# Kernel tuning notes

Hardware: AMD Instinct MI355X
Metric: run time of the kernel (lower is better)

The kernel has to match this reference:

```python
import jax, jax.numpy as jnp
import numpy as np

B, N, F, W = 8, 2048, 128, 64


def setup_inputs() -> dict:
    key = jax.random.key(0)
    k1, k2, k3, k4 = jax.random.split(key, 4)
    x = jax.random.normal(k1, (B, N, F), dtype=jnp.float32)
    adj = jnp.ones((B, N, N), dtype=bool)  # accepted by forward but unused
    w_key = jax.random.normal(k2, (F, W), dtype=jnp.float32) * 0.1
    w_value = jax.random.normal(k3, (F, F), dtype=jnp.float32) * 0.1
    w_query = jax.random.normal(k4, (F, W), dtype=jnp.float32) * 0.1
    return {"x": x, "adj": adj, "w_key": w_key, "w_value": w_value, "w_query": w_query}


def reference(x, adj, w_key, w_value, w_query):
    # keys/queries: [B, N, W]; values: [B, N, F]
    keys = x @ w_key
    querys = x @ w_query
    values = x @ w_value
    # per-batch softmax(Q K^T) over last dim -> [B, N, N]
    scores = jax.nn.softmax(jnp.einsum('bnw,bmw->bnm', querys, keys), axis=-1)
    # original broadcast-multiply-sum is exactly scores @ values
    out = jnp.einsum('bnm,bmf->bnf', scores, values)
    return out
```

## Files before the change

### kernel.cpp

```cpp
#include <hip/hip_runtime.h>
#include <hip/hip_bf16.h>
#include <math.h>

constexpr int B = 8;
constexpr int N = 2048;
constexpr int F = 128;
constexpr int W = 64;

constexpr int TQ = 128;
constexpr int TK = 64;
constexpr int KSPLIT = 4;
constexpr int TILES_PER_SPLIT = (N / TK) / KSPLIT;

typedef short     bf16x8 __attribute__((ext_vector_type(8)));
typedef _Float16  f16x8  __attribute__((ext_vector_type(8)));
typedef float     f32x4  __attribute__((ext_vector_type(4)));

__device__ inline ushort f2bf(float f) {
  union { float f; uint u; } v; v.f = f;
  uint u = v.u;
  return (ushort)((u + 0x7FFFu + ((u >> 16) & 1u)) >> 16);
}
__device__ inline float bf2f(ushort h) {
  union { uint u; float f; } v; v.u = ((uint)h) << 16;
  return v.f;
}

__device__ inline void lgkm_barrier() {
  asm volatile("s_waitcnt lgkmcnt(0)" ::: "memory");
  __builtin_amdgcn_s_barrier();
}

__global__ __launch_bounds__(256) void prep_w(
    const float* __restrict__ wq, const float* __restrict__ wk,
    const float* __restrict__ wv, _Float16* __restrict__ wt) {
  int gid = blockIdx.x * 256 + threadIdx.x;
  int n = gid >> 4;
  int k0 = (gid & 15) * 8;
  _Float16 t[8];
#pragma unroll
  for (int j = 0; j < 8; ++j) {
    int k = k0 + j;
    float val = (n < 64)  ? wq[k * W + n]
              : (n < 128) ? wk[k * W + (n - 64)]
                          : wv[k * F + (n - 128)];
    t[j] = (_Float16)val;
  }
  *(uint4*)&wt[n * 128 + k0] = *(uint4*)t;
}

constexpr int KP = 136;

__global__ __launch_bounds__(256) void proj_kernel(
    const float* __restrict__ x, const _Float16* __restrict__ wt,
    _Float16* __restrict__ q16, _Float16* __restrict__ k16,
    ushort* __restrict__ vt_ws) {
  __shared__ _Float16 xs[32][KP];

  const int tid  = threadIdx.x;
  const int wid  = tid >> 6;
  const int lane = tid & 63;
  const int lg = lane >> 4, li = lane & 15;
  const int pass = wid >> 1;
  const int rg   = wid & 1;
  const int brow0 = blockIdx.x * 32;
  const int b    = brow0 / N;
  const int nloc = brow0 % N;

  for (int idx = tid; idx < 32 * 128 / 4; idx += 256) {
    int row = idx >> 5, c4 = idx & 31;
    float4 xv = *(const float4*)&x[(size_t)(brow0 + row) * F + c4 * 4];
    _Float16 h[4] = {(_Float16)xv.x, (_Float16)xv.y,
                     (_Float16)xv.z, (_Float16)xv.w};
    *(float2*)&xs[row][c4 * 4] = *(float2*)h;
  }
  __syncthreads();

  f16x8 xa[4];
#pragma unroll
  for (int kk = 0; kk < 4; ++kk)
    xa[kk] = *(const f16x8*)&xs[rg * 16 + li][kk * 32 + lg * 8];

  f32x4 zero = {0.f, 0.f, 0.f, 0.f};
  f32x4 acc[8];
#pragma unroll
  for (int t = 0; t < 8; ++t) acc[t] = zero;

  const _Float16* wb = wt + (size_t)pass * 128 * 128;

  if (pass == 0) {
#pragma unroll
    for (int kk = 0; kk < 4; ++kk)
#pragma unroll
      for (int nt = 0; nt < 8; ++nt) {
        f16x8 bw = *(const f16x8*)&wb[(nt * 16 + li) * 128 + kk * 32 + lg * 8];
        acc[nt] = __builtin_amdgcn_mfma_f32_16x16x32_f16(xa[kk], bw, acc[nt], 0, 0, 0);
      }
#pragma unroll
    for (int nt = 0; nt < 8; ++nt)
#pragma unroll
      for (int r = 0; r < 4; ++r) {
        int row = brow0 + rg * 16 + lg * 4 + r;
        int c = nt * 16 + li;
        _Float16 hv = (_Float16)acc[nt][r];
        if (nt < 4) q16[row * W + c] = hv;
        else        k16[row * W + (c - 64)] = hv;
      }
  } else {
#pragma unroll
    for (int kk = 0; kk < 4; ++kk)
#pragma unroll
      for (int mt = 0; mt < 8; ++mt) {
        f16x8 aw = *(const f16x8*)&wb[(mt * 16 + li) * 128 + kk * 32 + lg * 8];
        acc[mt] = __builtin_amdgcn_mfma_f32_16x16x32_f16(aw, xa[kk], acc[mt], 0, 0, 0);
      }
#pragma unroll
    for (int mt = 0; mt < 8; ++mt)
#pragma unroll
      for (int r = 0; r < 4; ++r) {
        int f = mt * 16 + lg * 4 + r;
        int n = nloc + rg * 16 + li;
        vt_ws[(size_t)b * F * N + (size_t)f * N + n] = f2bf(acc[mt][r]);
      }
  }
}

constexpr int LP = 72;

__global__ __launch_bounds__(512) void attn_kernel(
    const _Float16* __restrict__ q16, const _Float16* __restrict__ k16,
    const ushort* __restrict__ vt_ws,
    ushort* __restrict__ op0, ushort* __restrict__ op1,
    ushort* __restrict__ op2, ushort* __restrict__ op3,
    float* __restrict__ lsums) {
  __shared__ _Float16 ksh[TK][LP];
  __shared__ ushort  vst[F][LP];
  __shared__ ushort  ps[8][16][LP];

  const int tid  = threadIdx.x;
  const int wid  = tid >> 6;
  const int lane = tid & 63;
  const int lg = lane >> 4, li = lane & 15;
  const int b = blockIdx.y, qt = blockIdx.x, split = blockIdx.z;

  const size_t koffb = (size_t)b * N * W;
  const ushort* vb = vt_ws + (size_t)b * F * N;

  const size_t qrow = (size_t)(b * N + qt * TQ + wid * 16 + li) * W;
  f16x8 qa[2];
  qa[0] = *(const f16x8*)&q16[qrow + lg * 8];
  qa[1] = *(const f16x8*)&q16[qrow + 32 + lg * 8];

  const int krow = tid >> 3, kc8 = tid & 7;
  const int vf0 = tid >> 3, vf1 = (tid + 512) >> 3;
  const int vc8 = tid & 7;

  uint4 kr, vr0, vr1;
  auto load_tile = [&](int kt) {
    kr  = *(const uint4*)&k16[koffb + (size_t)kt * TK * W + krow * W + kc8 * 8];
    vr0 = *(const uint4*)&vb[(size_t)vf0 * N + kt * TK + vc8 * 8];
    vr1 = *(const uint4*)&vb[(size_t)vf1 * N + kt * TK + vc8 * 8];
  };

  float l_lane = 0.f;
  f32x4 zero = {0.f, 0.f, 0.f, 0.f};
  f32x4 o_acc[8];
#pragma unroll
  for (int t = 0; t < 8; ++t) o_acc[t] = zero;

  const int kt0 = split * TILES_PER_SPLIT;
  load_tile(kt0);

  for (int kt = kt0; kt < kt0 + TILES_PER_SPLIT; ++kt) {
    lgkm_barrier();
    *(uint4*)&ksh[krow][kc8 * 8] = kr;
    *(uint4*)&vst[vf0][vc8 * 8] = vr0;
    *(uint4*)&vst[vf1][vc8 * 8] = vr1;
    if (kt + 1 < kt0 + TILES_PER_SPLIT) load_tile(kt + 1);
    lgkm_barrier();

    f32x4 s_acc[4];
#pragma unroll
    for (int nt = 0; nt < 4; ++nt) s_acc[nt] = zero;
#pragma unroll
    for (int kk = 0; kk < 2; ++kk)
#pragma unroll
      for (int nt = 0; nt < 4; ++nt) {
        f16x8 kf = *(const f16x8*)&ksh[nt * 16 + li][kk * 32 + lg * 8];
        s_acc[nt] = __builtin_amdgcn_mfma_f32_16x16x32_f16(kf, qa[kk], s_acc[nt], 0, 0, 0);
      }

#pragma unroll
    for (int nt = 0; nt < 4; ++nt) {
      ushort ph[4];
#pragma unroll
      for (int r = 0; r < 4; ++r) {
        float p = __expf(s_acc[nt][r]);
        ph[r] = f2bf(p);
        l_lane += bf2f(ph[r]);
      }
      *(float2*)&ps[wid][li][nt * 16 + lg * 4] = *(float2*)ph;
    }

#pragma unroll
    for (int kk = 0; kk < 2; ++kk) {
      bf16x8 pa = *(const bf16x8*)&ps[wid][li][kk * 32 + lg * 8];
#pragma unroll
      for (int ft = 0; ft < 8; ++ft) {
        bf16x8 vf = *(const bf16x8*)&vst[ft * 16 + li][kk * 32 + lg * 8];
        o_acc[ft] = __builtin_amdgcn_mfma_f32_16x16x32_bf16(pa, vf, o_acc[ft], 0, 0, 0);
      }
    }
  }

  l_lane += __shfl_xor(l_lane, 16, 64);
  l_lane += __shfl_xor(l_lane, 32, 64);

  ushort* opb = (split == 0) ? op0 : (split == 1) ? op1 : (split == 2) ? op2 : op3;
  ushort* ob = opb + (size_t)(b * N + qt * TQ) * F;
#pragma unroll
  for (int r = 0; r < 4; ++r) {
    int row = wid * 16 + lg * 4 + r;
#pragma unroll
    for (int ft = 0; ft < 8; ++ft)
      ob[row * F + ft * 16 + li] = f2bf(o_acc[ft][r]);
  }
  if (lg == 0) {
    size_t gr = (size_t)split * B * N + (size_t)(b * N + qt * TQ) + wid * 16 + li;
    lsums[gr] = l_lane;
  }
}

__global__ __launch_bounds__(256) void combine_kernel(
    const ushort* __restrict__ op0, const ushort* __restrict__ op1,
    const ushort* __restrict__ op2, const ushort* __restrict__ op3,
    const float* __restrict__ lsums, float* __restrict__ out) {
  const int gr  = blockIdx.x * 2 + (threadIdx.x >> 7);
  const int col = threadIdx.x & 127;
  constexpr size_t BN = (size_t)B * N;
  const float l = lsums[gr] + lsums[BN + gr] + lsums[2 * BN + gr] + lsums[3 * BN + gr];
  const float inv = 1.f / l;
  const size_t idx = (size_t)gr * F + col;
  out[idx] = (bf2f(op0[idx]) + bf2f(op1[idx]) + bf2f(op2[idx]) + bf2f(op3[idx])) * inv;
}

extern "C" void kernel_launch(void* const* d_in, const int* in_sizes, int n_in,
                              void* d_out, int out_size, void* d_ws, size_t ws_size,
                              hipStream_t stream) {
  const float* x  = (const float*)d_in[0];
  const float* wk = (const float*)d_in[2];
  const float* wv = (const float*)d_in[3];
  const float* wq = (const float*)d_in[4];
  float* out = (float*)d_out;

  constexpr size_t BNW = (size_t)B * N * W;
  constexpr size_t BNF = (size_t)B * N * F;
  _Float16* q16 = (_Float16*)d_ws;
  _Float16* k16 = q16 + BNW;
  ushort*   vt  = (ushort*)(k16 + BNW);
  _Float16* wt  = (_Float16*)(vt + BNF);
  ushort*   op0 = (ushort*)(wt + 32768);
  ushort*   op1 = op0 + BNF;
  ushort*   op2 = op1 + BNF;
  ushort*   op3 = op2 + BNF;
  float*    ls  = (float*)(op3 + BNF);

  prep_w<<<16, 256, 0, stream>>>(wq, wk, wv, wt);
  proj_kernel<<<(B * N) / 32, 256, 0, stream>>>(x, wt, q16, k16, vt);
  dim3 grid(N / TQ, B, KSPLIT);
  attn_kernel<<<grid, 512, 0, stream>>>(q16, k16, vt, op0, op1, op2, op3, ls);
  combine_kernel<<<B * N / 2, 256, 0, stream>>>(op0, op1, op2, op3, ls, out);
}
```

Baseline: 211.7 us.

## Pre-swizzle V into MFMA fragment layout and switch attention to 32x32 MFMA tiles

The projection kernel now writes V directly in the per-lane register fragment order used by 32x32x16 MFMAs. The attention kernel can then load V straight from global memory into registers, with no LDS staging. The attention kernel moves to 256-thread blocks with 32 query rows per wave, double-buffered K in LDS, a single barrier per tile, and a flattened grid remapped for locality. The combine kernel is vectorised to 8 elements per thread. This cuts LDS traffic and barriers, at the cost of more registers for the V fragments and reliance on the complex swizzled layout being correct.

```diff
diff --git a/kernel.cpp b/kernel.cpp
--- a/kernel.cpp
+++ b/kernel.cpp
@@ -15,6 +15,8 @@
 typedef short     bf16x8 __attribute__((ext_vector_type(8)));
 typedef _Float16  f16x8  __attribute__((ext_vector_type(8)));
 typedef float     f32x4  __attribute__((ext_vector_type(4)));
+typedef float     f32x16 __attribute__((ext_vector_type(16)));
+typedef ushort    u16x8  __attribute__((ext_vector_type(8)));
 
 __device__ inline ushort f2bf(float f) {
   union { float f; uint u; } v; v.f = f;
@@ -114,119 +116,144 @@
         f16x8 aw = *(const f16x8*)&wb[(mt * 16 + li) * 128 + kk * 32 + lg * 8];
         acc[mt] = __builtin_amdgcn_mfma_f32_16x16x32_f16(aw, xa[kk], acc[mt], 0, 0, 0);
       }
+    const int n   = nloc + rg * 16 + li;
+    const int kt  = n >> 6;
+    const int kk2 = (n >> 4) & 3;
+    const int fl  = ((n >> 3) & 1) * 32;
+    const int ei  = n & 7;
+    ushort* vb = vt_ws + (((size_t)(b * 32 + kt) * 4 + kk2) * 4) * 512;
 #pragma unroll
     for (int mt = 0; mt < 8; ++mt)
 #pragma unroll
       for (int r = 0; r < 4; ++r) {
         int f = mt * 16 + lg * 4 + r;
-        int n = nloc + rg * 16 + li;
-        vt_ws[(size_t)b * F * N + (size_t)f * N + n] = f2bf(acc[mt][r]);
-      }
-  }
-}
-
-constexpr int LP = 72;
-
-__global__ __launch_bounds__(512) void attn_kernel(
+        vb[(size_t)(f >> 5) * 512 + (size_t)(fl + (f & 31)) * 8 + ei] =
+            f2bf(acc[mt][r]);
+      }
+  }
+}
+
+constexpr int LK = 72;
+
+__global__ __launch_bounds__(256, 2) void attn_kernel(
     const _Float16* __restrict__ q16, const _Float16* __restrict__ k16,
-    const ushort* __restrict__ vt_ws,
+    const ushort* __restrict__ vfr,
     ushort* __restrict__ op0, ushort* __restrict__ op1,
     ushort* __restrict__ op2, ushort* __restrict__ op3,
     float* __restrict__ lsums) {
-  __shared__ _Float16 ksh[TK][LP];
-  __shared__ ushort  vst[F][LP];
-  __shared__ ushort  ps[8][16][LP];
+  __shared__ _Float16 ksh[2][TK][LK];
+  __shared__ ushort  ps[4][32][LK];
 
   const int tid  = threadIdx.x;
   const int wid  = tid >> 6;
   const int lane = tid & 63;
-  const int lg = lane >> 4, li = lane & 15;
-  const int b = blockIdx.y, qt = blockIdx.x, split = blockIdx.z;
+  const int q32  = lane & 31;
+  const int hi   = lane >> 5;
+
+  const int hw    = blockIdx.x;
+  const int grp   = (hw & 7) | ((hw >> 7) << 3);
+  const int qt    = (hw >> 3) & 15;
+  const int b     = grp & 7;
+  const int split = grp >> 3;
 
   const size_t koffb = (size_t)b * N * W;
-  const ushort* vb = vt_ws + (size_t)b * F * N;
-
-  const size_t qrow = (size_t)(b * N + qt * TQ + wid * 16 + li) * W;
-  f16x8 qa[2];
-  qa[0] = *(const f16x8*)&q16[qrow + lg * 8];
-  qa[1] = *(const f16x8*)&q16[qrow + 32 + lg * 8];
-
-  const int krow = tid >> 3, kc8 = tid & 7;
-  const int vf0 = tid >> 3, vf1 = (tid + 512) >> 3;
-  const int vc8 = tid & 7;
-
-  uint4 kr, vr0, vr1;
-  auto load_tile = [&](int kt) {
-    kr  = *(const uint4*)&k16[koffb + (size_t)kt * TK * W + krow * W + kc8 * 8];
-    vr0 = *(const uint4*)&vb[(size_t)vf0 * N + kt * TK + vc8 * 8];
-    vr1 = *(const uint4*)&vb[(size_t)vf1 * N + kt * TK + vc8 * 8];
+  const ushort* vfb_base = vfr + (size_t)b * 32 * 16 * 512;
+
+  const size_t qrow = (size_t)(b * N + qt * TQ + wid * 32 + q32) * W + hi * 8;
+  f16x8 qa[4];
+#pragma unroll
+  for (int kk = 0; kk < 4; ++kk)
+    qa[kk] = *(const f16x8*)&q16[qrow + kk * 16];
+
+  const int krow0 = tid >> 3, krow1 = krow0 + 32, kc8 = tid & 7;
+  uint4 kr0, kr1;
+  auto load_k = [&](int kt) {
+    kr0 = *(const uint4*)&k16[koffb + ((size_t)kt * TK + krow0) * W + kc8 * 8];
+    kr1 = *(const uint4*)&k16[koffb + ((size_t)kt * TK + krow1) * W + kc8 * 8];
   };
 
   float l_lane = 0.f;
-  f32x4 zero = {0.f, 0.f, 0.f, 0.f};
-  f32x4 o_acc[8];
-#pragma unroll
-  for (int t = 0; t < 8; ++t) o_acc[t] = zero;
+  f32x16 oa[4];
+#pragma unroll
+  for (int ft = 0; ft < 4; ++ft)
+#pragma unroll
+    for (int r = 0; r < 16; ++r) oa[ft][r] = 0.f;
 
   const int kt0 = split * TILES_PER_SPLIT;
-  load_tile(kt0);
-
-  for (int kt = kt0; kt < kt0 + TILES_PER_SPLIT; ++kt) {
+  load_k(kt0);
+
+  for (int t = 0; t < TILES_PER_SPLIT; ++t) {
+    const int kt = kt0 + t;
+    const int pb = t & 1;
+
+    const ushort* vfb = vfb_base + (size_t)kt * 16 * 512 + (size_t)lane * 8;
+    uint4 vreg[16];
+#pragma unroll
+    for (int kk2 = 0; kk2 < 4; ++kk2) {
+      const ushort* vb2 = vfb + kk2 * 2048;
+      vreg[kk2 * 4 + 0] = *(const uint4*)&vb2[0];
+      vreg[kk2 * 4 + 1] = *(const uint4*)&vb2[512];
+      vreg[kk2 * 4 + 2] = *(const uint4*)&vb2[1024];
+      vreg[kk2 * 4 + 3] = *(const uint4*)&vb2[1536];
+    }
+
+    *(uint4*)&ksh[pb][krow0][kc8 * 8] = kr0;
+    *(uint4*)&ksh[pb][krow1][kc8 * 8] = kr1;
+    if (t + 1 < TILES_PER_SPLIT) load_k(kt + 1);
+
     lgkm_barrier();
-    *(uint4*)&ksh[krow][kc8 * 8] = kr;
-    *(uint4*)&vst[vf0][vc8 * 8] = vr0;
-    *(uint4*)&vst[vf1][vc8 * 8] = vr1;
-    if (kt + 1 < kt0 + TILES_PER_SPLIT) load_tile(kt + 1);
-    lgkm_barrier();
-
-    f32x4 s_acc[4];
-#pragma unroll
-    for (int nt = 0; nt < 4; ++nt) s_acc[nt] = zero;
-#pragma unroll
-    for (int kk = 0; kk < 2; ++kk)
-#pragma unroll
-      for (int nt = 0; nt < 4; ++nt) {
-        f16x8 kf = *(const f16x8*)&ksh[nt * 16 + li][kk * 32 + lg * 8];
-        s_acc[nt] = __builtin_amdgcn_mfma_f32_16x16x32_f16(kf, qa[kk], s_acc[nt], 0, 0, 0);
-      }
-
-#pragma unroll
-    for (int nt = 0; nt < 4; ++nt) {
-      ushort ph[4];
-#pragma unroll
-      for (int r = 0; r < 4; ++r) {
-        float p = __expf(s_acc[nt][r]);
-        ph[r] = f2bf(p);
-        l_lane += bf2f(ph[r]);
-      }
-      *(float2*)&ps[wid][li][nt * 16 + lg * 4] = *(float2*)ph;
+
+    f32x16 s2[2];
+#pragma unroll
+    for (int mt = 0; mt < 2; ++mt)
+#pragma unroll
+      for (int r = 0; r < 16; ++r) s2[mt][r] = 0.f;
+#pragma unroll
+    for (int kk = 0; kk < 4; ++kk)
+#pragma unroll
+      for (int mt = 0; mt < 2; ++mt) {
+        f16x8 kf = *(const f16x8*)&ksh[pb][mt * 32 + q32][kk * 16 + hi * 8];
+        s2[mt] = __builtin_amdgcn_mfma_f32_32x32x16_f16(kf, qa[kk], s2[mt], 0, 0, 0);
+      }
+
+#pragma unroll
+    for (int mt = 0; mt < 2; ++mt)
+#pragma unroll
+      for (int gq = 0; gq < 4; ++gq) {
+        ushort ph[4];
+#pragma unroll
+        for (int j = 0; j < 4; ++j) {
+          float p = __expf(s2[mt][gq * 4 + j]);
+          ph[j] = f2bf(p);
+          l_lane += bf2f(ph[j]);
+        }
+        *(float2*)&ps[wid][q32][mt * 32 + gq * 8 + hi * 4] = *(float2*)ph;
+      }
+
+#pragma unroll
+    for (int kk2 = 0; kk2 < 4; ++kk2) {
+      bf16x8 pa = *(const bf16x8*)&ps[wid][q32][kk2 * 16 + hi * 8];
+#pragma unroll
+      for (int ft = 0; ft < 4; ++ft) {
+        bf16x8 vf = __builtin_bit_cast(bf16x8, vreg[kk2 * 4 + ft]);
+        oa[ft] = __builtin_amdgcn_mfma_f32_32x32x16_bf16(pa, vf, oa[ft], 0, 0, 0);
+      }
     }
-
-#pragma unroll
-    for (int kk = 0; kk < 2; ++kk) {
-      bf16x8 pa = *(const bf16x8*)&ps[wid][li][kk * 32 + lg * 8];
-#pragma unroll
-      for (int ft = 0; ft < 8; ++ft) {
-        bf16x8 vf = *(const bf16x8*)&vst[ft * 16 + li][kk * 32 + lg * 8];
-        o_acc[ft] = __builtin_amdgcn_mfma_f32_16x16x32_bf16(pa, vf, o_acc[ft], 0, 0, 0);
-      }
+  }
+
+  l_lane += __shfl_xor(l_lane, 32, 64);
+
+  ushort* opb = (split == 0) ? op0 : (split == 1) ? op1 : (split == 2) ? op2 : op3;
+  ushort* ob = opb + (size_t)(b * N + qt * TQ + wid * 32) * F;
+#pragma unroll
+  for (int ft = 0; ft < 4; ++ft)
+#pragma unroll
+    for (int r = 0; r < 16; ++r) {
+      int qr = (r & 3) + 8 * (r >> 2) + 4 * hi;
+      ob[(size_t)qr * F + ft * 32 + q32] = f2bf(oa[ft][r]);
     }
-  }
-
-  l_lane += __shfl_xor(l_lane, 16, 64);
-  l_lane += __shfl_xor(l_lane, 32, 64);
-
-  ushort* opb = (split == 0) ? op0 : (split == 1) ? op1 : (split == 2) ? op2 : op3;
-  ushort* ob = opb + (size_t)(b * N + qt * TQ) * F;
-#pragma unroll
-  for (int r = 0; r < 4; ++r) {
-    int row = wid * 16 + lg * 4 + r;
-#pragma unroll
-    for (int ft = 0; ft < 8; ++ft)
-      ob[row * F + ft * 16 + li] = f2bf(o_acc[ft][r]);
-  }
-  if (lg == 0) {
-    size_t gr = (size_t)split * B * N + (size_t)(b * N + qt * TQ) + wid * 16 + li;
+  if (hi == 0) {
+    size_t gr = (size_t)split * B * N + (size_t)(b * N + qt * TQ) + wid * 32 + q32;
     lsums[gr] = l_lane;
   }
 }
@@ -235,13 +262,23 @@
     const ushort* __restrict__ op0, const ushort* __restrict__ op1,
     const ushort* __restrict__ op2, const ushort* __restrict__ op3,
     const float* __restrict__ lsums, float* __restrict__ out) {
-  const int gr  = blockIdx.x * 2 + (threadIdx.x >> 7);
-  const int col = threadIdx.x & 127;
+  const int t  = blockIdx.x * 256 + threadIdx.x;
+  const int gr = t >> 4;
+  const int c8 = (t & 15) * 8;
   constexpr size_t BN = (size_t)B * N;
   const float l = lsums[gr] + lsums[BN + gr] + lsums[2 * BN + gr] + lsums[3 * BN + gr];
   const float inv = 1.f / l;
-  const size_t idx = (size_t)gr * F + col;
-  out[idx] = (bf2f(op0[idx]) + bf2f(op1[idx]) + bf2f(op2[idx]) + bf2f(op3[idx])) * inv;
+  const size_t base = (size_t)gr * F + c8;
+  u16x8 a0 = *(const u16x8*)&op0[base];
+  u16x8 a1 = *(const u16x8*)&op1[base];
+  u16x8 a2 = *(const u16x8*)&op2[base];
+  u16x8 a3 = *(const u16x8*)&op3[base];
+  float o[8];
+#pragma unroll
+  for (int j = 0; j < 8; ++j)
+    o[j] = (bf2f(a0[j]) + bf2f(a1[j]) + bf2f(a2[j]) + bf2f(a3[j])) * inv;
+  *(float4*)&out[base]     = *(float4*)&o[0];
+  *(float4*)&out[base + 4] = *(float4*)&o[4];
 }
 
 extern "C" void kernel_launch(void* const* d_in, const int* in_sizes, int n_in,
@@ -267,7 +304,6 @@
 
   prep_w<<<16, 256, 0, stream>>>(wq, wk, wv, wt);
   proj_kernel<<<(B * N) / 32, 256, 0, stream>>>(x, wt, q16, k16, vt);
-  dim3 grid(N / TQ, B, KSPLIT);
-  attn_kernel<<<grid, 512, 0, stream>>>(q16, k16, vt, op0, op1, op2, op3, ls);
-  combine_kernel<<<B * N / 2, 256, 0, stream>>>(op0, op1, op2, op3, ls, out);
-}
+  attn_kernel<<<dim3(512), 256, 0, stream>>>(q16, k16, vt, op0, op1, op2, op3, ls);
+  combine_kernel<<<(B * N * F / 8) / 256, 256, 0, stream>>>(op0, op1, op2, op3, ls, out);
+}
```

New measurement: 208.6 us. About the same (-1.5%).
